# Kernel optimization log

Hardware: AMD Instinct MI355X
Metric: run time of the kernel (lower is better)

## Reference

```python
import jax, jax.numpy as jnp
import numpy as np
import math

L, B, S, D, H, DFF, K_INDEX = 2, 32, 512, 512, 8, 2048, 5
DH = D // H  # 64


def setup_inputs() -> dict:
    key = jax.random.key(0)
    ks = jax.random.split(key, 10)
    rn = lambda k, shape, s=0.02: (s * jax.random.normal(k, shape)).astype(jnp.float32)
    return {
        "question_emb": jax.random.normal(ks[0], (B, S, D), jnp.float32),
        "interaction_emb": jax.random.normal(ks[1], (B, S, D), jnp.float32),
        "pos_emb": rn(ks[2], (1, S, D), 0.1),  # CosinePositionalEmbedding table (frozen, treated as input)
        "Wk": rn(ks[3], (L, D, D)), "bk": jnp.zeros((L, D), jnp.float32),  # kq_same=True: q and k share k_linear
        "Wv": rn(ks[4], (L, D, D)), "bv": jnp.zeros((L, D), jnp.float32),
        "Wo": rn(ks[5], (L, D, D)), "bo": jnp.zeros((L, D), jnp.float32),
        "ln1_g": jnp.ones((L, D), jnp.float32), "ln1_b": jnp.zeros((L, D), jnp.float32),
        "W1": rn(ks[6], (L, D, DFF)), "b1": jnp.zeros((L, DFF), jnp.float32),
        "W2": rn(ks[7], (L, DFF, D)), "b2": jnp.zeros((L, D), jnp.float32),
        "ln2_g": jnp.ones((L, D), jnp.float32), "ln2_b": jnp.zeros((L, D), jnp.float32),
    }


def layer_norm(x, g, b, eps=1e-5):
    m = jnp.mean(x, axis=-1, keepdims=True)
    v = jnp.var(x, axis=-1, keepdims=True)
    return (x - m) * jax.lax.rsqrt(v + eps) * g + b


def sparse_attention(q, k, v, keep_mask):
    # q,k,v: [B,H,S,DH]; keep_mask: [1,1,S,S] bool (strictly-causal, tril k=-1)
    scores = jnp.einsum('bhqd,bhkd->bhqk', q, k) / math.sqrt(DH)
    scores = jnp.where(keep_mask, scores, -1e32)
    scores = jax.nn.softmax(scores, axis=-1)
    scores = scores.at[:, :, 0, :].set(0.0)  # zero_pad=True: zero out first query row
    if K_INDEX + 1 < S:
        # SparseKT top-k: for rows > K_INDEX, keep only probs >= k-th largest, then re-softmax
        thresh = jax.lax.top_k(scores, K_INDEX)[0][..., -1:]  # k-th largest per row
        sparse = jnp.where(scores - thresh >= 0.0, scores, -1e16)
        sparse = jax.nn.softmax(sparse, axis=-1)
        row = jnp.arange(S)[None, None, :, None]
        scores = jnp.where(row <= K_INDEX, scores, sparse)
    return jnp.einsum('bhqk,bhkd->bhqd', scores, v)


def _forward(question_emb, interaction_emb, pos_emb, Wk, bk, Wv, bv, Wo, bo,
             ln1_g, ln1_b, W1, b1, W2, b2, ln2_g, ln2_b):
    x = question_emb + pos_emb[:, :S, :]
    y = interaction_emb + pos_emb[:, :S, :]
    keep_mask = jnp.tril(jnp.ones((S, S), bool), k=-1)[None, None]
    for l in range(L):
        def heads(t, W, b):
            return (t @ W + b).reshape(B, S, H, DH).transpose(0, 2, 1, 3)
        q = heads(x, Wk[l], bk[l])  # kq_same: q uses k_linear
        kk = heads(x, Wk[l], bk[l])
        vv = heads(y, Wv[l], bv[l])
        attn = sparse_attention(q, kk, vv, keep_mask)
        attn = attn.transpose(0, 2, 1, 3).reshape(B, S, D) @ Wo[l] + bo[l]
        x = layer_norm(x + attn, ln1_g[l], ln1_b[l])
        ff = jax.nn.relu(x @ W1[l] + b1[l]) @ W2[l] + b2[l]
        x = layer_norm(x + ff, ln2_g[l], ln2_b[l])
    return x


def reference(question_emb, interaction_emb, pos_emb, Wk, bk, Wv, bv, Wo, bo,
              ln1_g, ln1_b, W1, b1, W2, b2, ln2_g, ln2_b):
    return _forward(question_emb, interaction_emb, pos_emb, Wk, bk, Wv, bv, Wo, bo,
                    ln1_g, ln1_b, W1, b1, W2, b2, ln2_g, ln2_b)
```

## Files before the change

### kernel.cpp

```cpp
#include <hip/hip_runtime.h>


#define L_   2
#define B_   32
#define S_   512
#define D_   512
#define H_   8
#define DH_  64
#define DFF_ 2048
#define BS_  (B_*S_)

typedef __bf16 bfx8 __attribute__((ext_vector_type(8)));
typedef __bf16 bfx4 __attribute__((ext_vector_type(4)));
typedef float floatx4 __attribute__((ext_vector_type(4)));

__device__ __forceinline__ floatx4 mfma_bf16(bfx8 a, bfx8 b, floatx4 c) {
  return __builtin_amdgcn_mfma_f32_16x16x32_bf16(a, b, c, 0, 0, 0);
}

__device__ __forceinline__ float wave_sum(float v) {
  #pragma unroll
  for (int d = 32; d > 0; d >>= 1) v += __shfl_xor(v, d);
  return v;
}

__device__ __forceinline__ void lds_load16(__bf16* lds, const __bf16* g) {
  __builtin_amdgcn_global_load_lds(
      (const __attribute__((address_space(1))) unsigned int*)g,
      (__attribute__((address_space(3))) unsigned int*)lds, 16, 0, 0);
}

__device__ __forceinline__ int swz(int row, int q) { return q ^ ((row >> 1) & 3); }

__global__ void init_x_kernel(const float* __restrict__ qe, const float* __restrict__ pos,
                              __bf16* __restrict__ xh, __bf16* __restrict__ xl)
{
  size_t i = ((size_t)blockIdx.x * 256 + threadIdx.x) * 8;
  float4 a0 = *(const float4*)(qe + i);
  float4 a1 = *(const float4*)(qe + i + 4);
  size_t pi = i & (size_t)(S_*D_ - 1);
  float4 p0 = *(const float4*)(pos + pi);
  float4 p1 = *(const float4*)(pos + pi + 4);
  float v[8] = {a0.x+p0.x, a0.y+p0.y, a0.z+p0.z, a0.w+p0.w,
                a1.x+p1.x, a1.y+p1.y, a1.z+p1.z, a1.w+p1.w};
  bfx8 hv8, lv8;
  #pragma unroll
  for (int j = 0; j < 8; ++j) {
    __bf16 hv = (__bf16)v[j];
    hv8[j] = hv;
    lv8[j] = (__bf16)(v[j] - (float)hv);
  }
  *(bfx8*)(xh + i) = hv8;
  *(bfx8*)(xl + i) = lv8;
}

__global__ void transpose_split_kernel(const float* __restrict__ Wsrc,
                                       __bf16* __restrict__ Th, __bf16* __restrict__ Tl,
                                       int K, int N)
{
  __shared__ float tile[32][33];
  int n0 = blockIdx.x * 32, k0 = blockIdx.y * 32;
  int tx = threadIdx.x & 31, ty8 = threadIdx.x >> 5;
  #pragma unroll
  for (int j = 0; j < 4; ++j) {
    int k = ty8 + j*8;
    tile[k][tx] = Wsrc[(size_t)(k0 + k) * N + n0 + tx];
  }
  __syncthreads();
  #pragma unroll
  for (int j = 0; j < 4; ++j) {
    int n = ty8 + j*8;
    float vv = tile[tx][n];
    size_t dst = (size_t)(n0 + n) * K + k0 + tx;
    __bf16 hv = (__bf16)vv;
    Th[dst] = hv;
    Tl[dst] = (__bf16)(vv - (float)hv);
  }
}

__global__ __launch_bounds__(512, 4)
void gemm_split3_kernel(const __bf16* __restrict__ Ah, const __bf16* __restrict__ Al,
                        const float* __restrict__ Afa, const float* __restrict__ Afp,
                        const __bf16* __restrict__ Bth, const __bf16* __restrict__ Btl,
                        const float* __restrict__ bias,
                        __bf16* __restrict__ Ch, __bf16* __restrict__ Cl,
                        int M, int N, int K, int flags)
{
  __shared__ __bf16 sAh[2*128*32], sAl[2*128*32], sBh[2*128*32], sBl[2*128*32];
  const int t = threadIdx.x;
  const int w = t >> 6, lane = t & 63;
  const int q4 = lane >> 4, r16 = lane & 15;
  const int m0 = blockIdx.y * 128, n0 = blockIdx.x * 128;
  const int wr = (w >> 1) * 32, wc = (w & 1) * 64;

  floatx4 acc[2][4];
  #pragma unroll
  for (int i = 0; i < 2; ++i)
    #pragma unroll
    for (int j = 0; j < 4; ++j)
      acc[i][j] = (floatx4){0.f, 0.f, 0.f, 0.f};

  const int kind = w & 3, half = w >> 2;
  const __bf16* wsrc = (kind == 0) ? Ah : (kind == 1) ? Al : (kind == 2) ? Bth : Btl;
  __bf16* wdst = (kind == 0) ? sAh : (kind == 1) ? sAl : (kind == 2) ? sBh : sBl;
  const int rbase = ((kind < 2) ? m0 : n0) + half * 64;
  const int rl = lane >> 2;
  const int cp = lane & 3;

  const int srow = t >> 2;
  const int sq   = t & 3;

  auto stage = [&](int k0, int bo) {
    if (!(flags & 4)) {
      if ((flags & 2) && kind == 1) return;
      #pragma unroll
      for (int g = 0; g < 4; ++g) {
        int row = g*16 + rl;
        int qc = swz(half*64 + row, cp);
        const __bf16* gp = wsrc + (size_t)(rbase + row) * K + k0 + qc*8;
        lds_load16(wdst + bo + half*2048 + g*512, gp);
      }
    } else {
      int row = srow;
      size_t ga = (size_t)(m0 + row) * K + k0 + sq*8;
      size_t gp = (size_t)((m0 + row) & (S_ - 1)) * K + k0 + sq*8;
      float4 e0 = *(const float4*)&Afa[ga];
      float4 e1 = *(const float4*)&Afa[ga + 4];
      float4 p0 = *(const float4*)&Afp[gp];
      float4 p1 = *(const float4*)&Afp[gp + 4];
      float sv[8] = {e0.x+p0.x, e0.y+p0.y, e0.z+p0.z, e0.w+p0.w,
                     e1.x+p1.x, e1.y+p1.y, e1.z+p1.z, e1.w+p1.w};
      bfx8 hv8, lv8;
      #pragma unroll
      for (int j = 0; j < 8; ++j) {
        __bf16 hv = (__bf16)sv[j];
        hv8[j] = hv;
        lv8[j] = (__bf16)(sv[j] - (float)hv);
      }
      int pc = swz(row, sq);
      *(bfx8*)&sAh[bo + row*32 + pc*8] = hv8;
      *(bfx8*)&sAl[bo + row*32 + pc*8] = lv8;
      size_t gb = (size_t)(n0 + row) * K + k0 + sq*8;
      *(bfx8*)&sBh[bo + row*32 + pc*8] = *(const bfx8*)&Bth[gb];
      *(bfx8*)&sBl[bo + row*32 + pc*8] = *(const bfx8*)&Btl[gb];
    }
  };

  auto compute = [&](int bo) {
    bfx8 af[2][2], bfr[4][2];
    #pragma unroll
    for (int i = 0; i < 2; ++i) {
      int ar = wr + i*16 + r16;
      int sa = swz(ar, q4) * 8;
      af[i][0] = *(const bfx8*)&sAh[bo + ar*32 + sa];
      if (!(flags & 2)) af[i][1] = *(const bfx8*)&sAl[bo + ar*32 + sa];
    }
    #pragma unroll
    for (int j = 0; j < 4; ++j) {
      int br = wc + j*16 + r16;
      int sb = swz(br, q4) * 8;
      bfr[j][0] = *(const bfx8*)&sBh[bo + br*32 + sb];
      bfr[j][1] = *(const bfx8*)&sBl[bo + br*32 + sb];
    }
    __builtin_amdgcn_s_setprio(1);
    #pragma unroll
    for (int i = 0; i < 2; ++i)
      #pragma unroll
      for (int j = 0; j < 4; ++j) {
        acc[i][j] = mfma_bf16(af[i][0], bfr[j][0], acc[i][j]);
        acc[i][j] = mfma_bf16(af[i][0], bfr[j][1], acc[i][j]);
        if (!(flags & 2)) acc[i][j] = mfma_bf16(af[i][1], bfr[j][0], acc[i][j]);
      }
    __builtin_amdgcn_s_setprio(0);
  };

  const int nk = K >> 5;
  if (!(flags & 4)) {
    stage(0, 0);
    int bo = 0;
    for (int it = 0; it < nk; ++it) {
      if (it + 1 < nk) {
        stage((it + 1) << 5, bo ^ 4096);
        asm volatile("s_waitcnt vmcnt(4)" ::: "memory");
      } else {
        asm volatile("s_waitcnt vmcnt(0)" ::: "memory");
      }
      __builtin_amdgcn_s_barrier();
      __builtin_amdgcn_sched_barrier(0);
      compute(bo);
      __builtin_amdgcn_sched_barrier(0);
      __builtin_amdgcn_s_barrier();
      bo ^= 4096;
    }
  } else {
    stage(0, 0);
    __syncthreads();
    int bo = 0;
    for (int it = 0; it < nk; ++it) {
      if (it + 1 < nk) stage((it + 1) << 5, bo ^ 4096);
      compute(bo);
      __syncthreads();
      bo ^= 4096;
    }
  }

  #pragma unroll
  for (int i = 0; i < 2; ++i)
    #pragma unroll
    for (int j = 0; j < 4; ++j) {
      int gn = n0 + wc + j*16 + r16;
      float bb = bias[gn];
      #pragma unroll
      for (int r = 0; r < 4; ++r) {
        int gm = m0 + wr + i*16 + q4*4 + r;
        float val = acc[i][j][r] + bb;
        if (flags & 1) val = fmaxf(val, 0.f);
        size_t co = (size_t)gm * N + gn;
        __bf16 hv = (__bf16)val;
        Ch[co] = hv;
        if (!(flags & 8)) Cl[co] = (__bf16)(val - (float)hv);
      }
    }
}

template<int NJ>
__device__ __forceinline__ void attn_phase23(
    float* Ssc, const __bf16* __restrict__ vh, const __bf16* __restrict__ vl,
    __bf16* __restrict__ oh, __bf16* __restrict__ ol,
    int qt, int b, int hd, int w, int lane, int nkt)
{
  constexpr int LSS = 516;
  float p[4][NJ], mx[4], sm[4];
  #pragma unroll
  for (int rr = 0; rr < 4; ++rr) {
    const int lrow = w*4 + rr;
    float m = -3.0e38f;
    #pragma unroll
    for (int j = 0; j < NJ; ++j) {
      p[rr][j] = (j < nkt) ? Ssc[lrow*LSS + j*64 + lane] : -1e32f;
      m = fmaxf(m, p[rr][j]);
    }
    mx[rr] = m;
  }
  #pragma unroll
  for (int d = 32; d > 0; d >>= 1) {
    #pragma unroll
    for (int rr = 0; rr < 4; ++rr) mx[rr] = fmaxf(mx[rr], __shfl_xor(mx[rr], d));
  }
  #pragma unroll
  for (int rr = 0; rr < 4; ++rr) {
    float s = 0.f;
    #pragma unroll
    for (int j = 0; j < NJ; ++j) { p[rr][j] = __expf(p[rr][j] - mx[rr]); s += p[rr][j]; }
    sm[rr] = s;
  }
  #pragma unroll
  for (int d = 32; d > 0; d >>= 1) {
    #pragma unroll
    for (int rr = 0; rr < 4; ++rr) sm[rr] += __shfl_xor(sm[rr], d);
  }
  #pragma unroll
  for (int rr = 0; rr < 4; ++rr) {
    float inv = 1.0f / sm[rr];
    #pragma unroll
    for (int j = 0; j < NJ; ++j) p[rr][j] *= inv;
  }

  unsigned rm[4] = {0u, 0u, 0u, 0u};
  float pmax[4], thr[4];
  for (int it = 0; it < 5; ++it) {
    float loc[4]; int locj[4];
    #pragma unroll
    for (int rr = 0; rr < 4; ++rr) {
      loc[rr] = -1.f; locj[rr] = 0;
      #pragma unroll
      for (int j = 0; j < NJ; ++j)
        if (!((rm[rr] >> j) & 1u) && p[rr][j] > loc[rr]) { loc[rr] = p[rr][j]; locj[rr] = j; }
    }
    float wm4[4] = {loc[0], loc[1], loc[2], loc[3]};
    #pragma unroll
    for (int d = 32; d > 0; d >>= 1) {
      #pragma unroll
      for (int rr = 0; rr < 4; ++rr) wm4[rr] = fmaxf(wm4[rr], __shfl_xor(wm4[rr], d));
    }
    #pragma unroll
    for (int rr = 0; rr < 4; ++rr) {
      if (it == 0) pmax[rr] = wm4[rr];
      thr[rr] = wm4[rr];
      unsigned long long ball = __ballot(loc[rr] == wm4[rr]);
      int first = (int)__builtin_ctzll(ball);
      if (lane == first) rm[rr] |= 1u << locj[rr];
    }
  }

  float s2[4];
  #pragma unroll
  for (int rr = 0; rr < 4; ++rr) {
    const int grow = qt*16 + w*4 + rr;
    if (grow > 5) {
      float s = 0.f;
      #pragma unroll
      for (int j = 0; j < NJ; ++j) {
        float vv = (p[rr][j] - thr[rr] >= 0.f) ? __expf(p[rr][j] - pmax[rr]) : 0.f;
        p[rr][j] = vv; s += vv;
      }
      s2[rr] = s;
    } else {
      s2[rr] = 1.f;
    }
  }
  #pragma unroll
  for (int d = 32; d > 0; d >>= 1) {
    #pragma unroll
    for (int rr = 0; rr < 4; ++rr) s2[rr] += __shfl_xor(s2[rr], d);
  }

  const __bf16* vbh = vh + (size_t)b*S_*D_ + hd*64 + lane;
  const __bf16* vbl = vl + (size_t)b*S_*D_ + hd*64 + lane;
  #pragma unroll
  for (int rr = 0; rr < 4; ++rr) {
    const int lrow = w*4 + rr, grow = qt*16 + lrow;
    const float inv2 = 1.0f / s2[rr];
    float* Prow = &Ssc[lrow*LSS];
    unsigned long long msk[NJ];
    #pragma unroll
    for (int j = 0; j < NJ; ++j) {
      float f = (grow == 0) ? 0.f
              : (grow <= 5) ? p[rr][j]
              : p[rr][j] * inv2;
      Prow[j*64 + lane] = f;
      msk[j] = __ballot(f > 0.f);
    }
    float oacc = 0.f;
    #pragma unroll
    for (int j = 0; j < NJ; ++j) {
      unsigned long long m = msk[j];
      while (m) {
        int kk = (int)__builtin_ctzll(m); m &= m - 1;
        int key = j*64 + kk;
        float pv = Prow[j*64 + kk];
        size_t vo = (size_t)key * D_;
        float vv = (float)vbh[vo] + (float)vbl[vo];
        oacc = fmaf(pv, vv, oacc);
      }
    }
    size_t off = ((size_t)(b*S_ + grow)) * D_ + hd*64 + lane;
    __bf16 hv = (__bf16)oacc;
    oh[off] = hv;
    ol[off] = (__bf16)(oacc - (float)hv);
  }
}

__global__ __launch_bounds__(256, 4)
void attn_kernel(const __bf16* __restrict__ qh, const __bf16* __restrict__ ql,
                 const __bf16* __restrict__ vh, const __bf16* __restrict__ vl,
                 __bf16* __restrict__ oh, __bf16* __restrict__ ol)
{
  constexpr int LSS = 516;
  __shared__ float Ssc[16*LSS];
  const int lin = blockIdx.x;
  const int xcd = lin & 7;
  const int ord = lin >> 3;
  const int qt  = 31 - (ord & 31);
  const int bh  = ord >> 5;
  const int hd  = bh & 7;
  const int b   = ((bh >> 3) << 3) | xcd;
  const int t = threadIdx.x, w = t >> 6, lane = t & 63;
  const int q4 = lane >> 4, r16 = lane & 15;
  const int nkt = (qt >> 2) + 1;

  bfx8 qf[2][2];
  {
    size_t base = ((size_t)(b*S_ + qt*16 + r16)) * D_ + hd*64;
    #pragma unroll
    for (int ks = 0; ks < 2; ++ks) {
      qf[ks][0] = *(const bfx8*)&qh[base + ks*32 + q4*8];
      qf[ks][1] = *(const bfx8*)&ql[base + ks*32 + q4*8];
    }
  }

  bfx8 ch0, ch1, cl0, cl1, nh0, nh1, nl0, nl1;

  const size_t kstep = (size_t)64 * D_;
  const size_t kb0 = ((size_t)(b*S_ + w*16 + r16)) * D_ + hd*64 + q4*8;
  ch0 = *(const bfx8*)&qh[kb0];
  ch1 = *(const bfx8*)&qh[kb0 + 32];
  cl0 = *(const bfx8*)&ql[kb0];
  cl1 = *(const bfx8*)&ql[kb0 + 32];
  for (int kt = 0; kt < nkt; ++kt) {
    const bool more = (kt + 1 < nkt);
    if (more) {
      size_t nb = kb0 + (size_t)(kt + 1) * kstep;
      nh0 = *(const bfx8*)&qh[nb];
      nh1 = *(const bfx8*)&qh[nb + 32];
      nl0 = *(const bfx8*)&ql[nb];
      nl1 = *(const bfx8*)&ql[nb + 32];
    }
    floatx4 acc = (floatx4){0.f, 0.f, 0.f, 0.f};
    __builtin_amdgcn_s_setprio(1);
    acc = mfma_bf16(qf[0][0], ch0, acc);
    acc = mfma_bf16(qf[0][0], cl0, acc);
    acc = mfma_bf16(qf[0][1], ch0, acc);
    acc = mfma_bf16(qf[1][0], ch1, acc);
    acc = mfma_bf16(qf[1][0], cl1, acc);
    acc = mfma_bf16(qf[1][1], ch1, acc);
    __builtin_amdgcn_s_setprio(0);
    int gcol = kt*64 + w*16 + r16;
    #pragma unroll
    for (int r = 0; r < 4; ++r) {
      int lrow = q4*4 + r;
      int grow = qt*16 + lrow;
      float sc = acc[r] * 0.125f;
      if (gcol >= grow) sc = -1e32f;
      Ssc[lrow*LSS + gcol] = sc;
    }
    if (more) { ch0 = nh0; ch1 = nh1; cl0 = nl0; cl1 = nl1; }
  }
  __syncthreads();

  if (nkt <= 4) attn_phase23<4>(Ssc, vh, vl, oh, ol, qt, b, hd, w, lane, nkt);
  else          attn_phase23<8>(Ssc, vh, vl, oh, ol, qt, b, hd, w, lane, nkt);
}

__global__ void resid_ln_kernel(const __bf16* __restrict__ xhin, const __bf16* __restrict__ xlin,
                                const __bf16* __restrict__ thin, const __bf16* __restrict__ tlin,
                                const float* __restrict__ g, const float* __restrict__ bb,
                                __bf16* __restrict__ xh, __bf16* __restrict__ xl,
                                float* __restrict__ fout)
{
  int row = blockIdx.x * 4 + (threadIdx.x >> 6);
  int lane = threadIdx.x & 63;
  size_t base = (size_t)row * D_ + lane * 8;
  bfx8 h8 = *(const bfx8*)(xhin + base);
  bfx8 l8 = *(const bfx8*)(xlin + base);
  bfx8 th8 = *(const bfx8*)(thin + base);
  bfx8 tl8 = *(const bfx8*)(tlin + base);
  float v[8];
  #pragma unroll
  for (int j = 0; j < 8; ++j)
    v[j] = ((float)h8[j] + (float)l8[j]) + ((float)th8[j] + (float)tl8[j]);
  float s = 0.f;
  #pragma unroll
  for (int j = 0; j < 8; ++j) s += v[j];
  s = wave_sum(s);
  float mean = s * (1.0f/512.0f);
  float var = 0.f;
  #pragma unroll
  for (int j = 0; j < 8; ++j) { float d = v[j] - mean; var += d*d; }
  var = wave_sum(var) * (1.0f/512.0f);
  float rs = 1.0f / sqrtf(var + 1e-5f);
  float4 g0 = *(const float4*)(g + lane*8);
  float4 g1 = *(const float4*)(g + lane*8 + 4);
  float4 b0 = *(const float4*)(bb + lane*8);
  float4 b1 = *(const float4*)(bb + lane*8 + 4);
  float gg[8]  = {g0.x,g0.y,g0.z,g0.w,g1.x,g1.y,g1.z,g1.w};
  float bbv[8] = {b0.x,b0.y,b0.z,b0.w,b1.x,b1.y,b1.z,b1.w};
  float o[8];
  #pragma unroll
  for (int j = 0; j < 8; ++j) o[j] = (v[j] - mean) * rs * gg[j] + bbv[j];
  bfx8 hv8, lv8;
  #pragma unroll
  for (int j = 0; j < 8; ++j) {
    __bf16 hv = (__bf16)o[j];
    hv8[j] = hv;
    lv8[j] = (__bf16)(o[j] - (float)hv);
  }
  *(bfx8*)(xh + base) = hv8;
  *(bfx8*)(xl + base) = lv8;
  if (fout) {
    *(float4*)(fout + base)     = make_float4(o[0],o[1],o[2],o[3]);
    *(float4*)(fout + base + 4) = make_float4(o[4],o[5],o[6],o[7]);
  }
}

extern "C" void kernel_launch(void* const* d_in, const int* in_sizes, int n_in,
                              void* d_out, int out_size, void* d_ws, size_t ws_size,
                              hipStream_t stream)
{
  const float* qe   = (const float*)d_in[0];
  const float* ie   = (const float*)d_in[1];
  const float* pos  = (const float*)d_in[2];
  const float* Wk   = (const float*)d_in[3];
  const float* bk   = (const float*)d_in[4];
  const float* Wv   = (const float*)d_in[5];
  const float* bv   = (const float*)d_in[6];
  const float* Wo   = (const float*)d_in[7];
  const float* bo   = (const float*)d_in[8];
  const float* ln1g = (const float*)d_in[9];
  const float* ln1b = (const float*)d_in[10];
  const float* W1   = (const float*)d_in[11];
  const float* b1   = (const float*)d_in[12];
  const float* W2   = (const float*)d_in[13];
  const float* b2   = (const float*)d_in[14];
  const float* ln2g = (const float*)d_in[15];
  const float* ln2b = (const float*)d_in[16];

  char* wsp = (char*)d_ws;
  size_t off = 0;
  auto alloc = [&](size_t bytes) -> void* {
    void* p = wsp + off;
    off += (bytes + 255) & ~(size_t)255;
    return p;
  };
  const size_t NB = (size_t)BS_ * D_ * sizeof(__bf16);
  __bf16* xh  = (__bf16*)alloc(NB);
  __bf16* xl  = (__bf16*)alloc(NB);
  char*   qt_ = (char*)  alloc(2*NB);
  __bf16* qhb = (__bf16*)qt_;
  __bf16* qlb = (__bf16*)(qt_ + NB);
  __bf16* thb = (__bf16*)qt_;
  __bf16* tlb = (__bf16*)(qt_ + NB);
  __bf16* vhb = (__bf16*)alloc(NB);
  __bf16* vlb = (__bf16*)alloc(NB);
  char*   oh_ = (char*) alloc(2*NB);
  __bf16* ohb = (__bf16*)oh_;
  __bf16* olb = (__bf16*)(oh_ + NB);
  const size_t LW = 3*(size_t)D_*D_ + 2*(size_t)D_*DFF_;
  __bf16* wth = (__bf16*)alloc(2*LW*sizeof(__bf16));
  __bf16* wtl = (__bf16*)alloc(2*LW*sizeof(__bf16));
  __bf16* yh = (__bf16*)alloc(NB);
  __bf16* yl = (__bf16*)alloc(NB);
  const bool have_y = (off <= ws_size);
  __bf16* hhf = vhb;
  float*  xout = (float*)d_out;

  const size_t OK = 0, OV = (size_t)D_*D_, OO = 2*(size_t)D_*D_;
  const size_t O1 = 3*(size_t)D_*D_, O2 = 3*(size_t)D_*D_ + (size_t)D_*DFF_;

  for (int l = 0; l < L_; ++l) {
    size_t base = (size_t)l * LW;
    transpose_split_kernel<<<dim3(16,16), 256, 0, stream>>>(Wk + (size_t)l*D_*D_,   wth+base+OK, wtl+base+OK, D_,  D_);
    transpose_split_kernel<<<dim3(16,16), 256, 0, stream>>>(Wv + (size_t)l*D_*D_,   wth+base+OV, wtl+base+OV, D_,  D_);
    transpose_split_kernel<<<dim3(16,16), 256, 0, stream>>>(Wo + (size_t)l*D_*D_,   wth+base+OO, wtl+base+OO, D_,  D_);
    transpose_split_kernel<<<dim3(64,16), 256, 0, stream>>>(W1 + (size_t)l*D_*DFF_, wth+base+O1, wtl+base+O1, D_,  DFF_);
    transpose_split_kernel<<<dim3(16,64), 256, 0, stream>>>(W2 + (size_t)l*DFF_*D_, wth+base+O2, wtl+base+O2, DFF_, D_);
  }

  init_x_kernel<<<4096, 256, 0, stream>>>(qe, pos, xh, xl);
  if (have_y)
    init_x_kernel<<<4096, 256, 0, stream>>>(ie, pos, yh, yl);

  for (int l = 0; l < L_; ++l) {
    size_t base = (size_t)l * LW;
    gemm_split3_kernel<<<dim3(4,128), 512, 0, stream>>>(xh, xl, nullptr, nullptr,
        wth+base+OK, wtl+base+OK, bk + (size_t)l*D_, qhb, qlb, BS_, D_, D_, 0);
    if (have_y)
      gemm_split3_kernel<<<dim3(4,128), 512, 0, stream>>>(yh, yl, nullptr, nullptr,
          wth+base+OV, wtl+base+OV, bv + (size_t)l*D_, vhb, vlb, BS_, D_, D_, 0);
    else
      gemm_split3_kernel<<<dim3(4,128), 512, 0, stream>>>(nullptr, nullptr, ie, pos,
          wth+base+OV, wtl+base+OV, bv + (size_t)l*D_, vhb, vlb, BS_, D_, D_, 4);
    attn_kernel<<<dim3(32*H_*B_), 256, 0, stream>>>(qhb, qlb, vhb, vlb, ohb, olb);
    gemm_split3_kernel<<<dim3(4,128), 512, 0, stream>>>(ohb, olb, nullptr, nullptr,
        wth+base+OO, wtl+base+OO, bo + (size_t)l*D_, thb, tlb, BS_, D_, D_, 0);
    resid_ln_kernel<<<BS_/4, 256, 0, stream>>>(xh, xl, thb, tlb,
        ln1g + (size_t)l*D_, ln1b + (size_t)l*D_, xh, xl, nullptr);
    gemm_split3_kernel<<<dim3(16,128), 512, 0, stream>>>(xh, xl, nullptr, nullptr,
        wth+base+O1, wtl+base+O1, b1 + (size_t)l*DFF_, hhf, hhf, BS_, DFF_, D_, 1|8);
    gemm_split3_kernel<<<dim3(4,128), 512, 0, stream>>>(hhf, hhf, nullptr, nullptr,
        wth+base+O2, wtl+base+O2, b2 + (size_t)l*D_, thb, tlb, BS_, D_, DFF_, 2);
    resid_ln_kernel<<<BS_/4, 256, 0, stream>>>(xh, xl, thb, tlb,
        ln2g + (size_t)l*D_, ln2b + (size_t)l*D_, xh, xl,
        (l == L_-1) ? xout : nullptr);
  }
}
```

Baseline: 1.107 ms.

## Switch split-precision GEMMs to fp16 pairs and drop low weight parts

Changes the hi/lo split representation from bf16 to fp16 everywhere, so each half carries more mantissa bits. Most GEMMs now use only the high fp16 weight and skip the weight-low LDS tile and its MFMA, cutting loads, LDS space and MFMA work from three products to two. The GEMM is templated on flags so the unused paths are removed at compile time and the vmcnt wait matches the number of staged tiles. Risks are fp16 range overflow for large activations and lower accuracy from dropping the weight residual.

Result: faster. 1.020 ms (-7.9%).

```diff
diff --git a/kernel.cpp b/kernel.cpp
--- a/kernel.cpp
+++ b/kernel.cpp
@@ -10,12 +10,11 @@
 #define DFF_ 2048
 #define BS_  (B_*S_)
 
-typedef __bf16 bfx8 __attribute__((ext_vector_type(8)));
-typedef __bf16 bfx4 __attribute__((ext_vector_type(4)));
+typedef _Float16 hfx8 __attribute__((ext_vector_type(8)));
 typedef float floatx4 __attribute__((ext_vector_type(4)));
 
-__device__ __forceinline__ floatx4 mfma_bf16(bfx8 a, bfx8 b, floatx4 c) {
-  return __builtin_amdgcn_mfma_f32_16x16x32_bf16(a, b, c, 0, 0, 0);
+__device__ __forceinline__ floatx4 mfma_f16(hfx8 a, hfx8 b, floatx4 c) {
+  return __builtin_amdgcn_mfma_f32_16x16x32_f16(a, b, c, 0, 0, 0);
 }
 
 __device__ __forceinline__ float wave_sum(float v) {
@@ -24,7 +23,7 @@
   return v;
 }
 
-__device__ __forceinline__ void lds_load16(__bf16* lds, const __bf16* g) {
+__device__ __forceinline__ void lds_load16(_Float16* lds, const _Float16* g) {
   __builtin_amdgcn_global_load_lds(
       (const __attribute__((address_space(1))) unsigned int*)g,
       (__attribute__((address_space(3))) unsigned int*)lds, 16, 0, 0);
@@ -33,7 +32,7 @@
 __device__ __forceinline__ int swz(int row, int q) { return q ^ ((row >> 1) & 3); }
 
 __global__ void init_x_kernel(const float* __restrict__ qe, const float* __restrict__ pos,
-                              __bf16* __restrict__ xh, __bf16* __restrict__ xl)
+                              _Float16* __restrict__ xh, _Float16* __restrict__ xl)
 {
   size_t i = ((size_t)blockIdx.x * 256 + threadIdx.x) * 8;
   float4 a0 = *(const float4*)(qe + i);
@@ -43,19 +42,19 @@
   float4 p1 = *(const float4*)(pos + pi + 4);
   float v[8] = {a0.x+p0.x, a0.y+p0.y, a0.z+p0.z, a0.w+p0.w,
                 a1.x+p1.x, a1.y+p1.y, a1.z+p1.z, a1.w+p1.w};
-  bfx8 hv8, lv8;
+  hfx8 hv8, lv8;
   #pragma unroll
   for (int j = 0; j < 8; ++j) {
-    __bf16 hv = (__bf16)v[j];
+    _Float16 hv = (_Float16)v[j];
     hv8[j] = hv;
-    lv8[j] = (__bf16)(v[j] - (float)hv);
-  }
-  *(bfx8*)(xh + i) = hv8;
-  *(bfx8*)(xl + i) = lv8;
+    lv8[j] = (_Float16)(v[j] - (float)hv);
+  }
+  *(hfx8*)(xh + i) = hv8;
+  *(hfx8*)(xl + i) = lv8;
 }
 
 __global__ void transpose_split_kernel(const float* __restrict__ Wsrc,
-                                       __bf16* __restrict__ Th, __bf16* __restrict__ Tl,
+                                       _Float16* __restrict__ Th, _Float16* __restrict__ Tl,
                                        int K, int N)
 {
   __shared__ float tile[32][33];
@@ -72,21 +71,30 @@
     int n = ty8 + j*8;
     float vv = tile[tx][n];
     size_t dst = (size_t)(n0 + n) * K + k0 + tx;
-    __bf16 hv = (__bf16)vv;
+    _Float16 hv = (_Float16)vv;
     Th[dst] = hv;
-    Tl[dst] = (__bf16)(vv - (float)hv);
-  }
-}
-
+    Tl[dst] = (_Float16)(vv - (float)hv);
+  }
+}
+
+template<int FLAGS>
 __global__ __launch_bounds__(512, 4)
-void gemm_split3_kernel(const __bf16* __restrict__ Ah, const __bf16* __restrict__ Al,
-                        const float* __restrict__ Afa, const float* __restrict__ Afp,
-                        const __bf16* __restrict__ Bth, const __bf16* __restrict__ Btl,
-                        const float* __restrict__ bias,
-                        __bf16* __restrict__ Ch, __bf16* __restrict__ Cl,
-                        int M, int N, int K, int flags)
-{
-  __shared__ __bf16 sAh[2*128*32], sAl[2*128*32], sBh[2*128*32], sBl[2*128*32];
+void gemm_f16_kernel(const _Float16* __restrict__ Ah, const _Float16* __restrict__ Al,
+                     const float* __restrict__ Afa, const float* __restrict__ Afp,
+                     const _Float16* __restrict__ Bth, const _Float16* __restrict__ Btl,
+                     const float* __restrict__ bias,
+                     _Float16* __restrict__ Ch, _Float16* __restrict__ Cl,
+                     int M, int N, int K)
+{
+  constexpr bool A_PAIR = !(FLAGS & 2);
+  constexpr bool B_PAIR = (FLAGS & 16) != 0;
+  constexpr int KINDS = (A_PAIR ? 2 : 1) + (B_PAIR ? 2 : 1);
+  __shared__ _Float16 smem[KINDS * 2 * 4096];
+  _Float16* sAh = smem;
+  _Float16* sAl = A_PAIR ? smem + 8192 : smem;
+  _Float16* sBh = smem + (A_PAIR ? 16384 : 8192);
+  _Float16* sBl = B_PAIR ? smem + 24576 : smem;
+
   const int t = threadIdx.x;
   const int w = t >> 6, lane = t & 63;
   const int q4 = lane >> 4, r16 = lane & 15;
@@ -100,10 +108,6 @@
     for (int j = 0; j < 4; ++j)
       acc[i][j] = (floatx4){0.f, 0.f, 0.f, 0.f};
 
-  const int kind = w & 3, half = w >> 2;
-  const __bf16* wsrc = (kind == 0) ? Ah : (kind == 1) ? Al : (kind == 2) ? Bth : Btl;
-  __bf16* wdst = (kind == 0) ? sAh : (kind == 1) ? sAl : (kind == 2) ? sBh : sBl;
-  const int rbase = ((kind < 2) ? m0 : n0) + half * 64;
   const int rl = lane >> 2;
   const int cp = lane & 3;
 
@@ -111,14 +115,22 @@
   const int sq   = t & 3;
 
   auto stage = [&](int k0, int bo) {
-    if (!(flags & 4)) {
-      if ((flags & 2) && kind == 1) return;
-      #pragma unroll
-      for (int g = 0; g < 4; ++g) {
-        int row = g*16 + rl;
-        int qc = swz(half*64 + row, cp);
-        const __bf16* gp = wsrc + (size_t)(rbase + row) * K + k0 + qc*8;
-        lds_load16(wdst + bo + half*2048 + g*512, gp);
+    if constexpr (!(FLAGS & 4)) {
+      #pragma unroll
+      for (int c = 0; c < KINDS; ++c) {
+        const _Float16* src; _Float16* dst; int rbase;
+        if constexpr (A_PAIR) {
+          src = (c == 0) ? Ah : (c == 1) ? Al : (c == 2) ? Bth : Btl;
+          dst = (c == 0) ? sAh : (c == 1) ? sAl : (c == 2) ? sBh : sBl;
+          rbase = (c < 2) ? m0 : n0;
+        } else {
+          src = (c == 0) ? Ah : Bth;
+          dst = (c == 0) ? sAh : sBh;
+          rbase = (c == 0) ? m0 : n0;
+        }
+        int row = w*16 + rl;
+        int qc = swz(row, cp);
+        lds_load16(dst + bo + w*512, src + (size_t)(rbase + row) * K + k0 + qc*8);
       }
     } else {
       int row = srow;
@@ -130,58 +142,62 @@
       float4 p1 = *(const float4*)&Afp[gp + 4];
       float sv[8] = {e0.x+p0.x, e0.y+p0.y, e0.z+p0.z, e0.w+p0.w,
                      e1.x+p1.x, e1.y+p1.y, e1.z+p1.z, e1.w+p1.w};
-      bfx8 hv8, lv8;
+      hfx8 hv8, lv8;
       #pragma unroll
       for (int j = 0; j < 8; ++j) {
-        __bf16 hv = (__bf16)sv[j];
+        _Float16 hv = (_Float16)sv[j];
         hv8[j] = hv;
-        lv8[j] = (__bf16)(sv[j] - (float)hv);
+        lv8[j] = (_Float16)(sv[j] - (float)hv);
       }
       int pc = swz(row, sq);
-      *(bfx8*)&sAh[bo + row*32 + pc*8] = hv8;
-      *(bfx8*)&sAl[bo + row*32 + pc*8] = lv8;
+      *(hfx8*)&sAh[bo + row*32 + pc*8] = hv8;
+      *(hfx8*)&sAl[bo + row*32 + pc*8] = lv8;
       size_t gb = (size_t)(n0 + row) * K + k0 + sq*8;
-      *(bfx8*)&sBh[bo + row*32 + pc*8] = *(const bfx8*)&Bth[gb];
-      *(bfx8*)&sBl[bo + row*32 + pc*8] = *(const bfx8*)&Btl[gb];
+      *(hfx8*)&sBh[bo + row*32 + pc*8] = *(const hfx8*)&Bth[gb];
     }
   };
 
   auto compute = [&](int bo) {
-    bfx8 af[2][2], bfr[4][2];
+    hfx8 af[2][2], bfr[4][2];
     #pragma unroll
     for (int i = 0; i < 2; ++i) {
       int ar = wr + i*16 + r16;
       int sa = swz(ar, q4) * 8;
-      af[i][0] = *(const bfx8*)&sAh[bo + ar*32 + sa];
-      if (!(flags & 2)) af[i][1] = *(const bfx8*)&sAl[bo + ar*32 + sa];
+      af[i][0] = *(const hfx8*)&sAh[bo + ar*32 + sa];
+      if constexpr (A_PAIR) af[i][1] = *(const hfx8*)&sAl[bo + ar*32 + sa];
     }
     #pragma unroll
     for (int j = 0; j < 4; ++j) {
       int br = wc + j*16 + r16;
       int sb = swz(br, q4) * 8;
-      bfr[j][0] = *(const bfx8*)&sBh[bo + br*32 + sb];
-      bfr[j][1] = *(const bfx8*)&sBl[bo + br*32 + sb];
+      bfr[j][0] = *(const hfx8*)&sBh[bo + br*32 + sb];
+      if constexpr (B_PAIR) bfr[j][1] = *(const hfx8*)&sBl[bo + br*32 + sb];
     }
     __builtin_amdgcn_s_setprio(1);
     #pragma unroll
     for (int i = 0; i < 2; ++i)
       #pragma unroll
       for (int j = 0; j < 4; ++j) {
-        acc[i][j] = mfma_bf16(af[i][0], bfr[j][0], acc[i][j]);
-        acc[i][j] = mfma_bf16(af[i][0], bfr[j][1], acc[i][j]);
-        if (!(flags & 2)) acc[i][j] = mfma_bf16(af[i][1], bfr[j][0], acc[i][j]);
+        acc[i][j] = mfma_f16(af[i][0], bfr[j][0], acc[i][j]);
+        if constexpr (B_PAIR) acc[i][j] = mfma_f16(af[i][0], bfr[j][1], acc[i][j]);
+        if constexpr (A_PAIR) acc[i][j] = mfma_f16(af[i][1], bfr[j][0], acc[i][j]);
       }
     __builtin_amdgcn_s_setprio(0);
   };
 
   const int nk = K >> 5;
-  if (!(flags & 4)) {
+  if constexpr (!(FLAGS & 4)) {
     stage(0, 0);
     int bo = 0;
     for (int it = 0; it < nk; ++it) {
       if (it + 1 < nk) {
         stage((it + 1) << 5, bo ^ 4096);
-        asm volatile("s_waitcnt vmcnt(4)" ::: "memory");
+        if constexpr (KINDS == 4)
+          asm volatile("s_waitcnt vmcnt(4)" ::: "memory");
+        else if constexpr (KINDS == 3)
+          asm volatile("s_waitcnt vmcnt(3)" ::: "memory");
+        else
+          asm volatile("s_waitcnt vmcnt(2)" ::: "memory");
       } else {
         asm volatile("s_waitcnt vmcnt(0)" ::: "memory");
       }
@@ -214,19 +230,19 @@
       for (int r = 0; r < 4; ++r) {
         int gm = m0 + wr + i*16 + q4*4 + r;
         float val = acc[i][j][r] + bb;
-        if (flags & 1) val = fmaxf(val, 0.f);
+        if constexpr (FLAGS & 1) val = fmaxf(val, 0.f);
         size_t co = (size_t)gm * N + gn;
-        __bf16 hv = (__bf16)val;
+        _Float16 hv = (_Float16)val;
         Ch[co] = hv;
-        if (!(flags & 8)) Cl[co] = (__bf16)(val - (float)hv);
+        if constexpr (!(FLAGS & 8)) Cl[co] = (_Float16)(val - (float)hv);
       }
     }
 }
 
 template<int NJ>
 __device__ __forceinline__ void attn_phase23(
-    float* Ssc, const __bf16* __restrict__ vh, const __bf16* __restrict__ vl,
-    __bf16* __restrict__ oh, __bf16* __restrict__ ol,
+    float* Ssc, const _Float16* __restrict__ vh, const _Float16* __restrict__ vl,
+    _Float16* __restrict__ oh, _Float16* __restrict__ ol,
     int qt, int b, int hd, int w, int lane, int nkt)
 {
   constexpr int LSS = 516;
@@ -315,8 +331,8 @@
     for (int rr = 0; rr < 4; ++rr) s2[rr] += __shfl_xor(s2[rr], d);
   }
 
-  const __bf16* vbh = vh + (size_t)b*S_*D_ + hd*64 + lane;
-  const __bf16* vbl = vl + (size_t)b*S_*D_ + hd*64 + lane;
+  const _Float16* vbh = vh + (size_t)b*S_*D_ + hd*64 + lane;
+  const _Float16* vbl = vl + (size_t)b*S_*D_ + hd*64 + lane;
   #pragma unroll
   for (int rr = 0; rr < 4; ++rr) {
     const int lrow = w*4 + rr, grow = qt*16 + lrow;
@@ -345,16 +361,16 @@
       }
     }
     size_t off = ((size_t)(b*S_ + grow)) * D_ + hd*64 + lane;
-    __bf16 hv = (__bf16)oacc;
+    _Float16 hv = (_Float16)oacc;
     oh[off] = hv;
-    ol[off] = (__bf16)(oacc - (float)hv);
+    ol[off] = (_Float16)(oacc - (float)hv);
   }
 }
 
 __global__ __launch_bounds__(256, 4)
-void attn_kernel(const __bf16* __restrict__ qh, const __bf16* __restrict__ ql,
-                 const __bf16* __restrict__ vh, const __bf16* __restrict__ vl,
-                 __bf16* __restrict__ oh, __bf16* __restrict__ ol)
+void attn_kernel(const _Float16* __restrict__ qh, const _Float16* __restrict__ ql,
+                 const _Float16* __restrict__ vh, const _Float16* __restrict__ vl,
+                 _Float16* __restrict__ oh, _Float16* __restrict__ ol)
 {
   constexpr int LSS = 516;
   __shared__ float Ssc[16*LSS];
@@ -369,41 +385,41 @@
   const int q4 = lane >> 4, r16 = lane & 15;
   const int nkt = (qt >> 2) + 1;
 
-  bfx8 qf[2][2];
+  hfx8 qf[2][2];
   {
     size_t base = ((size_t)(b*S_ + qt*16 + r16)) * D_ + hd*64;
     #pragma unroll
     for (int ks = 0; ks < 2; ++ks) {
-      qf[ks][0] = *(const bfx8*)&qh[base + ks*32 + q4*8];
-      qf[ks][1] = *(const bfx8*)&ql[base + ks*32 + q4*8];
-    }
-  }
-
-  bfx8 ch0, ch1, cl0, cl1, nh0, nh1, nl0, nl1;
+      qf[ks][0] = *(const hfx8*)&qh[base + ks*32 + q4*8];
+      qf[ks][1] = *(const hfx8*)&ql[base + ks*32 + q4*8];
+    }
+  }
+
+  hfx8 ch0, ch1, cl0, cl1, nh0, nh1, nl0, nl1;
 
   const size_t kstep = (size_t)64 * D_;
   const size_t kb0 = ((size_t)(b*S_ + w*16 + r16)) * D_ + hd*64 + q4*8;
-  ch0 = *(const bfx8*)&qh[kb0];
-  ch1 = *(const bfx8*)&qh[kb0 + 32];
-  cl0 = *(const bfx8*)&ql[kb0];
-  cl1 = *(const bfx8*)&ql[kb0 + 32];
+  ch0 = *(const hfx8*)&qh[kb0];
+  ch1 = *(const hfx8*)&qh[kb0 + 32];
+  cl0 = *(const hfx8*)&ql[kb0];
+  cl1 = *(const hfx8*)&ql[kb0 + 32];
   for (int kt = 0; kt < nkt; ++kt) {
     const bool more = (kt + 1 < nkt);
     if (more) {
       size_t nb = kb0 + (size_t)(kt + 1) * kstep;
-      nh0 = *(const bfx8*)&qh[nb];
-      nh1 = *(const bfx8*)&qh[nb + 32];
-      nl0 = *(const bfx8*)&ql[nb];
-      nl1 = *(const bfx8*)&ql[nb + 32];
+      nh0 = *(const hfx8*)&qh[nb];
+      nh1 = *(const hfx8*)&qh[nb + 32];
+      nl0 = *(const hfx8*)&ql[nb];
+      nl1 = *(const hfx8*)&ql[nb + 32];
     }
     floatx4 acc = (floatx4){0.f, 0.f, 0.f, 0.f};
     __builtin_amdgcn_s_setprio(1);
-    acc = mfma_bf16(qf[0][0], ch0, acc);
-    acc = mfma_bf16(qf[0][0], cl0, acc);
-    acc = mfma_bf16(qf[0][1], ch0, acc);
-    acc = mfma_bf16(qf[1][0], ch1, acc);
-    acc = mfma_bf16(qf[1][0], cl1, acc);
-    acc = mfma_bf16(qf[1][1], ch1, acc);
+    acc = mfma_f16(qf[0][0], ch0, acc);
+    acc = mfma_f16(qf[0][0], cl0, acc);
+    acc = mfma_f16(qf[0][1], ch0, acc);
+    acc = mfma_f16(qf[1][0], ch1, acc);
+    acc = mfma_f16(qf[1][0], cl1, acc);
+    acc = mfma_f16(qf[1][1], ch1, acc);
     __builtin_amdgcn_s_setprio(0);
     int gcol = kt*64 + w*16 + r16;
     #pragma unroll
@@ -422,19 +438,19 @@
   else          attn_phase23<8>(Ssc, vh, vl, oh, ol, qt, b, hd, w, lane, nkt);
 }
 
-__global__ void resid_ln_kernel(const __bf16* __restrict__ xhin, const __bf16* __restrict__ xlin,
-                                const __bf16* __restrict__ thin, const __bf16* __restrict__ tlin,
+__global__ void resid_ln_kernel(const _Float16* __restrict__ xhin, const _Float16* __restrict__ xlin,
+                                const _Float16* __restrict__ thin, const _Float16* __restrict__ tlin,
                                 const float* __restrict__ g, const float* __restrict__ bb,
-                                __bf16* __restrict__ xh, __bf16* __restrict__ xl,
+                                _Float16* __restrict__ xh, _Float16* __restrict__ xl,
                                 float* __restrict__ fout)
 {
   int row = blockIdx.x * 4 + (threadIdx.x >> 6);
   int lane = threadIdx.x & 63;
   size_t base = (size_t)row * D_ + lane * 8;
-  bfx8 h8 = *(const bfx8*)(xhin + base);
-  bfx8 l8 = *(const bfx8*)(xlin + base);
-  bfx8 th8 = *(const bfx8*)(thin + base);
-  bfx8 tl8 = *(const bfx8*)(tlin + base);
+  hfx8 h8 = *(const hfx8*)(xhin + base);
+  hfx8 l8 = *(const hfx8*)(xlin + base);
+  hfx8 th8 = *(const hfx8*)(thin + base);
+  hfx8 tl8 = *(const hfx8*)(tlin + base);
   float v[8];
   #pragma unroll
   for (int j = 0; j < 8; ++j)
@@ -458,15 +474,15 @@
   float o[8];
   #pragma unroll
   for (int j = 0; j < 8; ++j) o[j] = (v[j] - mean) * rs * gg[j] + bbv[j];
-  bfx8 hv8, lv8;
+  hfx8 hv8, lv8;
   #pragma unroll
   for (int j = 0; j < 8; ++j) {
-    __bf16 hv = (__bf16)o[j];
+    _Float16 hv = (_Float16)o[j];
     hv8[j] = hv;
-    lv8[j] = (__bf16)(o[j] - (float)hv);
-  }
-  *(bfx8*)(xh + base) = hv8;
-  *(bfx8*)(xl + base) = lv8;
+    lv8[j] = (_Float16)(o[j] - (float)hv);
+  }
+  *(hfx8*)(xh + base) = hv8;
+  *(hfx8*)(xl + base) = lv8;
   if (fout) {
     *(float4*)(fout + base)     = make_float4(o[0],o[1],o[2],o[3]);
     *(float4*)(fout + base + 4) = make_float4(o[4],o[5],o[6],o[7]);
@@ -502,26 +518,26 @@
     off += (bytes + 255) & ~(size_t)255;
     return p;
   };
-  const size_t NB = (size_t)BS_ * D_ * sizeof(__bf16);
-  __bf16* xh  = (__bf16*)alloc(NB);
-  __bf16* xl  = (__bf16*)alloc(NB);
-  char*   qt_ = (char*)  alloc(2*NB);
-  __bf16* qhb = (__bf16*)qt_;
-  __bf16* qlb = (__bf16*)(qt_ + NB);
-  __bf16* thb = (__bf16*)qt_;
-  __bf16* tlb = (__bf16*)(qt_ + NB);
-  __bf16* vhb = (__bf16*)alloc(NB);
-  __bf16* vlb = (__bf16*)alloc(NB);
-  char*   oh_ = (char*) alloc(2*NB);
-  __bf16* ohb = (__bf16*)oh_;
-  __bf16* olb = (__bf16*)(oh_ + NB);
+  const size_t NB = (size_t)BS_ * D_ * sizeof(_Float16);
+  _Float16* xh  = (_Float16*)alloc(NB);
+  _Float16* xl  = (_Float16*)alloc(NB);
+  char*     qt_ = (char*)  alloc(2*NB);
+  _Float16* qhb = (_Float16*)qt_;
+  _Float16* qlb = (_Float16*)(qt_ + NB);
+  _Float16* thb = (_Float16*)qt_;
+  _Float16* tlb = (_Float16*)(qt_ + NB);
+  _Float16* vhb = (_Float16*)alloc(NB);
+  _Float16* vlb = (_Float16*)alloc(NB);
+  char*     oh_ = (char*) alloc(2*NB);
+  _Float16* ohb = (_Float16*)oh_;
+  _Float16* olb = (_Float16*)(oh_ + NB);
   const size_t LW = 3*(size_t)D_*D_ + 2*(size_t)D_*DFF_;
-  __bf16* wth = (__bf16*)alloc(2*LW*sizeof(__bf16));
-  __bf16* wtl = (__bf16*)alloc(2*LW*sizeof(__bf16));
-  __bf16* yh = (__bf16*)alloc(NB);
-  __bf16* yl = (__bf16*)alloc(NB);
+  _Float16* wth = (_Float16*)alloc(2*LW*sizeof(_Float16));
+  _Float16* wtl = (_Float16*)alloc(2*LW*sizeof(_Float16));
+  _Float16* yh = (_Float16*)alloc(NB);
+  _Float16* yl = (_Float16*)alloc(NB);
   const bool have_y = (off <= ws_size);
-  __bf16* hhf = vhb;
+  _Float16* hhf = vhb;
   float*  xout = (float*)d_out;
 
   const size_t OK = 0, OV = (size_t)D_*D_, OO = 2*(size_t)D_*D_;
@@ -542,23 +558,23 @@
 
   for (int l = 0; l < L_; ++l) {
     size_t base = (size_t)l * LW;
-    gemm_split3_kernel<<<dim3(4,128), 512, 0, stream>>>(xh, xl, nullptr, nullptr,
-        wth+base+OK, wtl+base+OK, bk + (size_t)l*D_, qhb, qlb, BS_, D_, D_, 0);
+    gemm_f16_kernel<16><<<dim3(4,128), 512, 0, stream>>>(xh, xl, nullptr, nullptr,
+        wth+base+OK, wtl+base+OK, bk + (size_t)l*D_, qhb, qlb, BS_, D_, D_);
     if (have_y)
-      gemm_split3_kernel<<<dim3(4,128), 512, 0, stream>>>(yh, yl, nullptr, nullptr,
-          wth+base+OV, wtl+base+OV, bv + (size_t)l*D_, vhb, vlb, BS_, D_, D_, 0);
+      gemm_f16_kernel<0><<<dim3(4,128), 512, 0, stream>>>(yh, yl, nullptr, nullptr,
+          wth+base+OV, wtl+base+OV, bv + (size_t)l*D_, vhb, vlb, BS_, D_, D_);
     else
-      gemm_split3_kernel<<<dim3(4,128), 512, 0, stream>>>(nullptr, nullptr, ie, pos,
-          wth+base+OV, wtl+base+OV, bv + (size_t)l*D_, vhb, vlb, BS_, D_, D_, 4);
+      gemm_f16_kernel<4><<<dim3(4,128), 512, 0, stream>>>(nullptr, nullptr, ie, pos,
+          wth+base+OV, wtl+base+OV, bv + (size_t)l*D_, vhb, vlb, BS_, D_, D_);
     attn_kernel<<<dim3(32*H_*B_), 256, 0, stream>>>(qhb, qlb, vhb, vlb, ohb, olb);
-    gemm_split3_kernel<<<dim3(4,128), 512, 0, stream>>>(ohb, olb, nullptr, nullptr,
-        wth+base+OO, wtl+base+OO, bo + (size_t)l*D_, thb, tlb, BS_, D_, D_, 0);
+    gemm_f16_kernel<0><<<dim3(4,128), 512, 0, stream>>>(ohb, olb, nullptr, nullptr,
+        wth+base+OO, wtl+base+OO, bo + (size_t)l*D_, thb, tlb, BS_, D_, D_);
     resid_ln_kernel<<<BS_/4, 256, 0, stream>>>(xh, xl, thb, tlb,
         ln1g + (size_t)l*D_, ln1b + (size_t)l*D_, xh, xl, nullptr);
-    gemm_split3_kernel<<<dim3(16,128), 512, 0, stream>>>(xh, xl, nullptr, nullptr,
-        wth+base+O1, wtl+base+O1, b1 + (size_t)l*DFF_, hhf, hhf, BS_, DFF_, D_, 1|8);
-    gemm_split3_kernel<<<dim3(4,128), 512, 0, stream>>>(hhf, hhf, nullptr, nullptr,
-        wth+base+O2, wtl+base+O2, b2 + (size_t)l*D_, thb, tlb, BS_, D_, DFF_, 2);
+    gemm_f16_kernel<1|8><<<dim3(16,128), 512, 0, stream>>>(xh, xl, nullptr, nullptr,
+        wth+base+O1, wtl+base+O1, b1 + (size_t)l*DFF_, hhf, hhf, BS_, DFF_, D_);
+    gemm_f16_kernel<2><<<dim3(4,128), 512, 0, stream>>>(hhf, hhf, nullptr, nullptr,
+        wth+base+O2, wtl+base+O2, b2 + (size_t)l*D_, thb, tlb, BS_, D_, DFF_);
     resid_ln_kernel<<<BS_/4, 256, 0, stream>>>(xh, xl, thb, tlb,
         ln2g + (size_t)l*D_, ln2b + (size_t)l*D_, xh, xl,
         (l == L_-1) ? xout : nullptr);
```
